# Kernel optimization log

Measured on AMD Instinct MI355X. Metric: run time of the kernel, lower is better.

Reference implementation:

```python
import jax, jax.numpy as jnp
import numpy as np

HIDDEN = 1024
HEADS = 16
HEAD_DIM = HIDDEN // HEADS
B, S = 4, 2048


def setup_inputs() -> dict:
    key = jax.random.key(0)
    ks = jax.random.split(key, 10)
    scale = 1.0 / np.sqrt(HIDDEN)
    def lin(k):
        return jax.random.uniform(k, (HIDDEN, HIDDEN), jnp.float32, -scale, scale)
    return {
        "x": jax.random.normal(ks[0], (B, S, HIDDEN), jnp.float32),
        "Wq": lin(ks[1]), "bq": jnp.zeros((HIDDEN,), jnp.float32),
        "Wk": lin(ks[2]), "bk": jnp.zeros((HIDDEN,), jnp.float32),
        "Wv": lin(ks[3]), "bv": jnp.zeros((HIDDEN,), jnp.float32),
        "Wo": lin(ks[4]), "bo": jnp.zeros((HIDDEN,), jnp.float32),
        "head_mask": jnp.ones((HEADS,), jnp.float32),
    }


def reference(x, Wq, bq, Wk, bk, Wv, bv, Wo, bo, head_mask):
    b, s, _ = x.shape
    # torch Linear: x @ W.T + b
    q = (x @ Wq.T + bq).reshape(b, s, HEADS, HEAD_DIM)
    k = (x @ Wk.T + bk).reshape(b, s, HEADS, HEAD_DIM)
    v = (x @ Wv.T + bv).reshape(b, s, HEADS, HEAD_DIM)
    # [b, h, s, s] attention scores
    attn = jnp.einsum("bqhd,bkhd->bhqk", q, k) / np.sqrt(HEAD_DIM).astype(np.float32)
    attn = jax.nn.softmax(attn, axis=-1)
    # post-softmax per-head mask scaling
    attn = attn * head_mask[None, :, None, None]
    out = jnp.einsum("bhqk,bkhd->bqhd", attn, v).reshape(b, s, HIDDEN)
    return out @ Wo.T + bo
```

## Files before the change

kernel.cpp:

```cpp
#include <hip/hip_runtime.h>
#include <hip/hip_bf16.h>

typedef __attribute__((ext_vector_type(8))) short bf16x8;
typedef __attribute__((ext_vector_type(4))) float f32x4;

#define SEQ 2048
#define NB 4
#define NH 16
#define HID 1024

__device__ __forceinline__ short f2bf(float f) {
  __hip_bfloat16 h = __float2bfloat16(f);
  union { __hip_bfloat16 h; short s; } u; u.h = h; return u.s;
}

__device__ __forceinline__ void gload_lds16(const void* g, void* l) {
  __builtin_amdgcn_global_load_lds((const __attribute__((address_space(1))) void*)g,
                                   (__attribute__((address_space(3))) void*)l, 16, 0, 0);
}

__global__ void cvt_f32_bf16(const float4* __restrict__ in, short4* __restrict__ out, int n4) {
  int i = blockIdx.x * 256 + threadIdx.x;
  if (i >= n4) return;
  float4 v = in[i];
  short4 o;
  o.x = f2bf(v.x); o.y = f2bf(v.y); o.z = f2bf(v.z); o.w = f2bf(v.w);
  out[i] = o;
}

template<int MODE>
__global__ __launch_bounds__(256, 2)
void gemm_bf16(const short* __restrict__ A,
               const short* __restrict__ B0, const short* __restrict__ B1, const short* __restrict__ B2,
               const float* __restrict__ bias0, const float* __restrict__ bias1, const float* __restrict__ bias2,
               short* __restrict__ o0, short* __restrict__ o1, short* __restrict__ o2,
               float* __restrict__ of) {
  __shared__ __align__(16) short As[128*64];
  __shared__ __align__(16) short Bs[128*64];
  const int tid = threadIdx.x;
  const int wave = tid >> 6, lane = tid & 63;
  const int lr = lane & 15, lk = lane >> 4;
  const int m0 = blockIdx.y * 128;
  const int n0 = blockIdx.x * 128;

  const short* Bm; const float* bias; int nloc; int proj = 0;
  if (MODE == 0) {
    proj = n0 >> 10;
    Bm   = proj == 0 ? B0 : (proj == 1 ? B1 : B2);
    bias = proj == 0 ? bias0 : (proj == 1 ? bias1 : bias2);
    nloc = n0 & 1023;
  } else { Bm = B0; bias = bias0; nloc = n0; }

  f32x4 acc[4][4];
  #pragma unroll
  for (int m = 0; m < 4; ++m)
    #pragma unroll
    for (int n = 0; n < 4; ++n) acc[m][n] = (f32x4){0.f,0.f,0.f,0.f};

  const int wr = (wave >> 1) * 64, wc = (wave & 1) * 64;

  for (int kt = 0; kt < 1024; kt += 64) {
    #pragma unroll
    for (int is = 0; is < 4; ++is) {
      int slot = is*256 + tid;
      int r = slot >> 3;
      int cs = (slot & 7) ^ (r & 7);
      gload_lds16(A  + (m0  + r)*1024 + kt + cs*8, As + (is*256 + wave*64)*8);
      gload_lds16(Bm + (nloc+ r)*1024 + kt + cs*8, Bs + (is*256 + wave*64)*8);
    }
    __syncthreads();
    #pragma unroll
    for (int kk = 0; kk < 2; ++kk) {
      bf16x8 av[4], bv[4];
      #pragma unroll
      for (int m = 0; m < 4; ++m) {
        int r = wr + m*16 + lr;
        av[m] = *(const bf16x8*)(As + (r*8 + ((kk*4 + lk) ^ (r & 7)))*8);
      }
      #pragma unroll
      for (int n = 0; n < 4; ++n) {
        int r = wc + n*16 + lr;
        bv[n] = *(const bf16x8*)(Bs + (r*8 + ((kk*4 + lk) ^ (r & 7)))*8);
      }
      #pragma unroll
      for (int m = 0; m < 4; ++m)
        #pragma unroll
        for (int n = 0; n < 4; ++n)
          acc[m][n] = __builtin_amdgcn_mfma_f32_16x16x32_bf16(av[m], bv[n], acc[m][n], 0, 0, 0);
    }
    __syncthreads();
  }

  if (MODE == 0) {
    if (proj < 2) {
      short* outp = proj == 0 ? o0 : o1;
      const float scale = (proj == 0) ? 0.125f : 1.0f;
      #pragma unroll
      for (int n = 0; n < 4; ++n) {
        int col = nloc + wc + n*16 + lr;
        int h = col >> 6, d = col & 63;
        float bvv = bias[col];
        #pragma unroll
        for (int m = 0; m < 4; ++m)
          #pragma unroll
          for (int j = 0; j < 4; ++j) {
            int row = m0 + wr + m*16 + lk*4 + j;
            int b = row >> 11, s = row & 2047;
            outp[(((b*NH + h)*SEQ + s) << 6) + d] = f2bf((acc[m][n][j] + bvv) * scale);
          }
      }
    } else {
      #pragma unroll
      for (int n = 0; n < 4; ++n) {
        int col = nloc + wc + n*16 + lr;
        int h = col >> 6, d = col & 63;
        float bvv = bias[col];
        #pragma unroll
        for (int m = 0; m < 4; ++m) {
          int row = m0 + wr + m*16 + lk*4;
          int b = row >> 11, s = row & 2047;
          short4 vv;
          vv.x = f2bf(acc[m][n][0] + bvv);
          vv.y = f2bf(acc[m][n][1] + bvv);
          vv.z = f2bf(acc[m][n][2] + bvv);
          vv.w = f2bf(acc[m][n][3] + bvv);
          *(short4*)(o2 + (((b*NH + h)*64 + d)*SEQ + s)) = vv;
        }
      }
    }
  } else {
    #pragma unroll
    for (int n = 0; n < 4; ++n) {
      int col = n0 + wc + n*16 + lr;
      float bvv = bias[col];
      #pragma unroll
      for (int m = 0; m < 4; ++m)
        #pragma unroll
        for (int j = 0; j < 4; ++j) {
          int row = m0 + wr + m*16 + lk*4 + j;
          of[row*HID + col] = acc[m][n][j] + bvv;
        }
    }
  }
}

__global__ __launch_bounds__(256, 2)
void attn_fwd(const short* __restrict__ Q, const short* __restrict__ K,
              const short* __restrict__ VT, const float* __restrict__ head_mask,
              short* __restrict__ O) {
  __shared__ __align__(16) short Ks[64*64];
  __shared__ __align__(16) short Vs[64*64];
  __shared__ __align__(16) short Ps[4][16*64];
  const int tid = threadIdx.x;
  const int wave = tid >> 6, lane = tid & 63;
  const int lr = lane & 15, lk = lane >> 4;
  const int bh = blockIdx.y;
  const int h = bh & (NH - 1);
  const int q0 = blockIdx.x * 64;
  const short* Qh = Q  + bh * SEQ * 64;
  const short* Kh = K  + bh * SEQ * 64;
  const short* Vh = VT + bh * 64 * SEQ;

  bf16x8 qf[2];
  {
    const short* qr = Qh + (q0 + wave*16 + lr)*64 + lk*8;
    qf[0] = *(const bf16x8*)qr;
    qf[1] = *(const bf16x8*)(qr + 32);
  }

  float row_m[4], row_l[4];
  f32x4 oacc[4];
  #pragma unroll
  for (int j = 0; j < 4; ++j) { row_m[j] = -1e30f; row_l[j] = 0.f; }
  #pragma unroll
  for (int n = 0; n < 4; ++n) oacc[n] = (f32x4){0.f,0.f,0.f,0.f};

  for (int kv0 = 0; kv0 < SEQ; kv0 += 64) {
    #pragma unroll
    for (int is = 0; is < 2; ++is) {
      int slot = is*256 + tid;
      int r = slot >> 3;
      int cs = (slot & 7) ^ (r & 7);
      gload_lds16(Kh + (kv0 + r)*64 + cs*8, Ks + (is*256 + wave*64)*8);
      gload_lds16(Vh + r*SEQ + kv0 + cs*8, Vs + (is*256 + wave*64)*8);
    }
    __syncthreads();

    f32x4 sc[4];
    #pragma unroll
    for (int n = 0; n < 4; ++n) sc[n] = (f32x4){0.f,0.f,0.f,0.f};
    #pragma unroll
    for (int kk = 0; kk < 2; ++kk)
      #pragma unroll
      for (int n = 0; n < 4; ++n) {
        int r = n*16 + lr;
        bf16x8 bv = *(const bf16x8*)(Ks + (r*8 + ((kk*4 + lk) ^ (r & 7)))*8);
        sc[n] = __builtin_amdgcn_mfma_f32_16x16x32_bf16(qf[kk], bv, sc[n], 0, 0, 0);
      }

    float pmax[4];
    #pragma unroll
    for (int j = 0; j < 4; ++j) {
      float v = fmaxf(fmaxf(sc[0][j], sc[1][j]), fmaxf(sc[2][j], sc[3][j]));
      v = fmaxf(v, __shfl_xor(v, 1));
      v = fmaxf(v, __shfl_xor(v, 2));
      v = fmaxf(v, __shfl_xor(v, 4));
      v = fmaxf(v, __shfl_xor(v, 8));
      pmax[j] = v;
    }
    float ps[4], rs[4];
    #pragma unroll
    for (int j = 0; j < 4; ++j) {
      float mn = fmaxf(row_m[j], pmax[j]);
      ps[j] = __expf(row_m[j] - mn);
      row_m[j] = mn;
      rs[j] = 0.f;
    }
    #pragma unroll
    for (int n = 0; n < 4; ++n)
      #pragma unroll
      for (int j = 0; j < 4; ++j) {
        float p = __expf(sc[n][j] - row_m[j]);
        sc[n][j] = p;
        rs[j] += p;
      }
    #pragma unroll
    for (int j = 0; j < 4; ++j) {
      float v = rs[j];
      v += __shfl_xor(v, 1);
      v += __shfl_xor(v, 2);
      v += __shfl_xor(v, 4);
      v += __shfl_xor(v, 8);
      row_l[j] = row_l[j]*ps[j] + v;
    }
    #pragma unroll
    for (int n = 0; n < 4; ++n)
      #pragma unroll
      for (int j = 0; j < 4; ++j) oacc[n][j] *= ps[j];

    short* Pw = Ps[wave];
    #pragma unroll
    for (int n = 0; n < 4; ++n)
      #pragma unroll
      for (int j = 0; j < 4; ++j) {
        int row = lk*4 + j;
        int col = n*16 + lr;
        int byteoff = row*128 + (((col >> 3) ^ (row >> 1))*16) + (col & 7)*2;
        *(short*)((char*)Pw + byteoff) = f2bf(sc[n][j]);
      }
    __syncthreads();

    #pragma unroll
    for (int kk = 0; kk < 2; ++kk) {
      bf16x8 av = *(const bf16x8*)(Pw + (lr*8 + ((kk*4 + lk) ^ (lr >> 1)))*8);
      #pragma unroll
      for (int n = 0; n < 4; ++n) {
        int r = n*16 + lr;
        bf16x8 bv = *(const bf16x8*)(Vs + (r*8 + ((kk*4 + lk) ^ (r & 7)))*8);
        oacc[n] = __builtin_amdgcn_mfma_f32_16x16x32_bf16(av, bv, oacc[n], 0, 0, 0);
      }
    }
    __syncthreads();
  }

  const float hm = head_mask[h];
  const int b = bh >> 4;
  #pragma unroll
  for (int j = 0; j < 4; ++j) {
    int q = q0 + wave*16 + lk*4 + j;
    float inv = hm / row_l[j];
    int rowbase = (b*SEQ + q)*HID + h*64;
    #pragma unroll
    for (int n = 0; n < 4; ++n)
      O[rowbase + n*16 + lr] = f2bf(oacc[n][j] * inv);
  }
}

extern "C" void kernel_launch(void* const* d_in, const int* in_sizes, int n_in,
                              void* d_out, int out_size, void* d_ws, size_t ws_size,
                              hipStream_t stream) {
  const float* x  = (const float*)d_in[0];
  const float* Wq = (const float*)d_in[1];
  const float* bq = (const float*)d_in[2];
  const float* Wk = (const float*)d_in[3];
  const float* bk = (const float*)d_in[4];
  const float* Wv = (const float*)d_in[5];
  const float* bv = (const float*)d_in[6];
  const float* Wo = (const float*)d_in[7];
  const float* bo = (const float*)d_in[8];
  const float* hm = (const float*)d_in[9];
  float* out = (float*)d_out;
  char* ws = (char*)d_ws;

  short* xb  = (short*)(ws);
  short* wqb = (short*)(ws + 16777216);
  short* wkb = (short*)(ws + 18874368);
  short* wvb = (short*)(ws + 20971520);
  short* wob = (short*)(ws + 23068672);
  short* Qb  = (short*)(ws + 25165824);
  short* Kb  = (short*)(ws + 41943040);
  short* Vb  = (short*)(ws + 58720256);
  short* AOb = (short*)(ws + 75497472);

  cvt_f32_bf16<<<8192, 256, 0, stream>>>((const float4*)x,  (short4*)xb,  2097152);
  cvt_f32_bf16<<<1024, 256, 0, stream>>>((const float4*)Wq, (short4*)wqb, 262144);
  cvt_f32_bf16<<<1024, 256, 0, stream>>>((const float4*)Wk, (short4*)wkb, 262144);
  cvt_f32_bf16<<<1024, 256, 0, stream>>>((const float4*)Wv, (short4*)wvb, 262144);
  cvt_f32_bf16<<<1024, 256, 0, stream>>>((const float4*)Wo, (short4*)wob, 262144);

  gemm_bf16<0><<<dim3(24, 64), 256, 0, stream>>>(xb, wqb, wkb, wvb, bq, bk, bv,
                                                 Qb, Kb, Vb, nullptr);
  attn_fwd<<<dim3(32, 64), 256, 0, stream>>>(Qb, Kb, Vb, hm, AOb);
  gemm_bf16<1><<<dim3(8, 64), 256, 0, stream>>>(AOb, wob, nullptr, nullptr, bo, nullptr, nullptr,
                                                nullptr, nullptr, nullptr, out);
}
```

Before: 392.5 us.

## Double-buffer K/V tiles, lazy softmax rescale, and drop intra-iteration barrier

K/V tiles are now double-buffered in LDS: the next tile's global-to-LDS load is issued before computing on the current one, so memory latency overlaps the MFMA work. The online softmax skips rescaling the accumulators unless some row max grows by more than 8 (wave-uniform check), which saves exp and multiply work. The barrier between the per-wave P store and the PV MFMA is removed, since each wave reads only its own P tile, and launch bounds rise to 4 blocks per CU. The extra LDS per block and the higher occupancy target could force register spills or limit residency, and the lazy rescale lets unnormalized values grow up to e^8.

```diff
diff --git a/kernel.cpp b/kernel.cpp
--- a/kernel.cpp
+++ b/kernel.cpp
@@ -144,12 +144,12 @@
   }
 }
 
-__global__ __launch_bounds__(256, 2)
+__global__ __launch_bounds__(256, 4)
 void attn_fwd(const short* __restrict__ Q, const short* __restrict__ K,
               const short* __restrict__ VT, const float* __restrict__ head_mask,
               short* __restrict__ O) {
-  __shared__ __align__(16) short Ks[64*64];
-  __shared__ __align__(16) short Vs[64*64];
+  __shared__ __align__(16) short Ks[2][64*64];
+  __shared__ __align__(16) short Vs[2][64*64];
   __shared__ __align__(16) short Ps[4][16*64];
   const int tid = threadIdx.x;
   const int wave = tid >> 6, lane = tid & 63;
@@ -161,6 +161,17 @@
   const short* Kh = K  + bh * SEQ * 64;
   const short* Vh = VT + bh * 64 * SEQ;
 
+  auto STAGE = [&](int buf, int kv0) {
+    #pragma unroll
+    for (int is = 0; is < 2; ++is) {
+      int slot = is*256 + tid;
+      int r = slot >> 3;
+      int cs = (slot & 7) ^ (r & 7);
+      gload_lds16(Kh + (kv0 + r)*64 + cs*8, Ks[buf] + (is*256 + wave*64)*8);
+      gload_lds16(Vh + r*SEQ + kv0 + cs*8, Vs[buf] + (is*256 + wave*64)*8);
+    }
+  };
+
   bf16x8 qf[2];
   {
     const short* qr = Qh + (q0 + wave*16 + lr)*64 + lk*8;
@@ -175,16 +186,13 @@
   #pragma unroll
   for (int n = 0; n < 4; ++n) oacc[n] = (f32x4){0.f,0.f,0.f,0.f};
 
-  for (int kv0 = 0; kv0 < SEQ; kv0 += 64) {
-    #pragma unroll
-    for (int is = 0; is < 2; ++is) {
-      int slot = is*256 + tid;
-      int r = slot >> 3;
-      int cs = (slot & 7) ^ (r & 7);
-      gload_lds16(Kh + (kv0 + r)*64 + cs*8, Ks + (is*256 + wave*64)*8);
-      gload_lds16(Vh + r*SEQ + kv0 + cs*8, Vs + (is*256 + wave*64)*8);
-    }
-    __syncthreads();
+  STAGE(0, 0);
+  __syncthreads();
+
+  const int NT = SEQ / 64;
+  for (int t = 0; t < NT; ++t) {
+    const int cur = t & 1;
+    if (t + 1 < NT) STAGE(cur ^ 1, (t + 1) * 64);
 
     f32x4 sc[4];
     #pragma unroll
@@ -194,7 +202,7 @@
       #pragma unroll
       for (int n = 0; n < 4; ++n) {
         int r = n*16 + lr;
-        bf16x8 bv = *(const bf16x8*)(Ks + (r*8 + ((kk*4 + lk) ^ (r & 7)))*8);
+        bf16x8 bv = *(const bf16x8*)(Ks[cur] + (r*8 + ((kk*4 + lk) ^ (r & 7)))*8);
         sc[n] = __builtin_amdgcn_mfma_f32_16x16x32_bf16(qf[kk], bv, sc[n], 0, 0, 0);
       }
 
@@ -208,14 +216,20 @@
       v = fmaxf(v, __shfl_xor(v, 8));
       pmax[j] = v;
     }
-    float ps[4], rs[4];
-    #pragma unroll
-    for (int j = 0; j < 4; ++j) {
-      float mn = fmaxf(row_m[j], pmax[j]);
-      ps[j] = __expf(row_m[j] - mn);
-      row_m[j] = mn;
-      rs[j] = 0.f;
-    }
+    bool ok = (pmax[0] <= row_m[0] + 8.f) && (pmax[1] <= row_m[1] + 8.f) &&
+              (pmax[2] <= row_m[2] + 8.f) && (pmax[3] <= row_m[3] + 8.f);
+    if (!__all(ok)) {
+      #pragma unroll
+      for (int j = 0; j < 4; ++j) {
+        float mn = fmaxf(row_m[j], pmax[j]);
+        float ps = __expf(row_m[j] - mn);
+        row_m[j] = mn;
+        row_l[j] *= ps;
+        #pragma unroll
+        for (int n = 0; n < 4; ++n) oacc[n][j] *= ps;
+      }
+    }
+    float rs[4] = {0.f, 0.f, 0.f, 0.f};
     #pragma unroll
     for (int n = 0; n < 4; ++n)
       #pragma unroll
@@ -231,12 +245,8 @@
       v += __shfl_xor(v, 2);
       v += __shfl_xor(v, 4);
       v += __shfl_xor(v, 8);
-      row_l[j] = row_l[j]*ps[j] + v;
-    }
-    #pragma unroll
-    for (int n = 0; n < 4; ++n)
-      #pragma unroll
-      for (int j = 0; j < 4; ++j) oacc[n][j] *= ps[j];
+      row_l[j] += v;
+    }
 
     short* Pw = Ps[wave];
     #pragma unroll
@@ -248,7 +258,6 @@
         int byteoff = row*128 + (((col >> 3) ^ (row >> 1))*16) + (col & 7)*2;
         *(short*)((char*)Pw + byteoff) = f2bf(sc[n][j]);
       }
-    __syncthreads();
 
     #pragma unroll
     for (int kk = 0; kk < 2; ++kk) {
@@ -256,7 +265,7 @@
       #pragma unroll
       for (int n = 0; n < 4; ++n) {
         int r = n*16 + lr;
-        bf16x8 bv = *(const bf16x8*)(Vs + (r*8 + ((kk*4 + lk) ^ (r & 7)))*8);
+        bf16x8 bv = *(const bf16x8*)(Vs[cur] + (r*8 + ((kk*4 + lk) ^ (r & 7)))*8);
         oacc[n] = __builtin_amdgcn_mfma_f32_16x16x32_bf16(av, bv, oacc[n], 0, 0, 0);
       }
     }
```

Result: slower. 416.3 us (+6.1%).

## Restructure attention with 32x32 MFMA, transposed scores, double-buffered KV, register P

Applied to the files above, without the earlier changes.

Rewrites the flash-attention kernel to process 128 query rows per block using 32x32x16 MFMAs, computing S^T so each lane owns one query row and softmax reductions become mostly in-register. K/V tiles are double-buffered in LDS and prefetched one tile ahead. P is repacked through lane shuffles instead of an LDS round trip, which drops one barrier per tile. Rescaling of the output accumulator is skipped unless the running max grows by more than 8. This adds register pressure and more complex lane mapping, and halves the grid size.

```diff
diff --git a/kernel.cpp b/kernel.cpp
--- a/kernel.cpp
+++ b/kernel.cpp
@@ -3,15 +3,22 @@
 
 typedef __attribute__((ext_vector_type(8))) short bf16x8;
 typedef __attribute__((ext_vector_type(4))) float f32x4;
+typedef __attribute__((ext_vector_type(16))) float f32x16;
+typedef unsigned int u32;
 
 #define SEQ 2048
 #define NB 4
 #define NH 16
 #define HID 1024
+#define QBLK 128
 
 __device__ __forceinline__ short f2bf(float f) {
   __hip_bfloat16 h = __float2bfloat16(f);
   union { __hip_bfloat16 h; short s; } u; u.h = h; return u.s;
+}
+
+__device__ __forceinline__ u32 pk2(float a, float b) {
+  return (u32)(unsigned short)f2bf(a) | ((u32)(unsigned short)f2bf(b) << 16);
 }
 
 __device__ __forceinline__ void gload_lds16(const void* g, void* l) {
@@ -144,135 +151,165 @@
   }
 }
 
-__global__ __launch_bounds__(256, 2)
+
+template<int BUF>
+__device__ __forceinline__ void attn_stage(int tid, int wave,
+                                           const short* __restrict__ Kh,
+                                           const short* __restrict__ Vh, int kv0,
+                                           short (&Ks)[2][64*64], short (&Vs)[2][64*64]) {
+  #pragma unroll
+  for (int is = 0; is < 2; ++is) {
+    int slot = is*256 + tid;
+    int r = slot >> 3;
+    int cs = (slot & 7) ^ (r & 7);
+    gload_lds16(Kh + (kv0 + r)*64 + cs*8, Ks[BUF] + (is*256 + wave*64)*8);
+    gload_lds16(Vh + r*SEQ + kv0 + cs*8, Vs[BUF] + (is*256 + wave*64)*8);
+  }
+}
+
+template<int CUR>
+__device__ __forceinline__ void attn_tile(int t, int NT, int tid, int wave, int qq, int hi,
+                                          const short* __restrict__ Kh,
+                                          const short* __restrict__ Vh,
+                                          short (&Ks)[2][64*64], short (&Vs)[2][64*64],
+                                          bf16x8 (&qf)[4], float& row_m, float& row_l,
+                                          f32x16 (&oacc)[2]) {
+  if (t + 1 < NT) attn_stage<CUR ^ 1>(tid, wave, Kh, Vh, (t + 1) * 64, Ks, Vs);
+
+  f32x16 sc[2];
+  #pragma unroll
+  for (int i = 0; i < 16; ++i) { sc[0][i] = 0.f; sc[1][i] = 0.f; }
+  #pragma unroll
+  for (int kb = 0; kb < 2; ++kb) {
+    int r = kb*32 + qq;
+    #pragma unroll
+    for (int ks = 0; ks < 4; ++ks) {
+      bf16x8 ka = *(const bf16x8*)(Ks[CUR] + (r*8 + ((ks*2 + hi) ^ (r & 7)))*8);
+      sc[kb] = __builtin_amdgcn_mfma_f32_32x32x16_bf16(ka, qf[ks], sc[kb], 0, 0, 0);
+    }
+  }
+
+  float tm[16];
+  #pragma unroll
+  for (int i = 0; i < 16; ++i) tm[i] = fmaxf(sc[0][i], sc[1][i]);
+  #pragma unroll
+  for (int s = 8; s >= 1; s >>= 1)
+    #pragma unroll
+    for (int i = 0; i < s; ++i) tm[i] = fmaxf(tm[i], tm[i + s]);
+  float mt = fmaxf(tm[0], __shfl_xor(tm[0], 32));
+
+  if (__any(mt > row_m + 8.f)) {
+    float mn = fmaxf(row_m, mt);
+    float ps = __expf(row_m - mn);
+    row_m = mn;
+    row_l *= ps;
+    #pragma unroll
+    for (int rg = 0; rg < 16; ++rg) {
+      int qsrc = (rg & 3) + 8*(rg >> 2) + 4*hi;
+      float po = __shfl(ps, qsrc);
+      oacc[0][rg] *= po;
+      oacc[1][rg] *= po;
+    }
+  }
+
+  #pragma unroll
+  for (int kb = 0; kb < 2; ++kb)
+    #pragma unroll
+    for (int i = 0; i < 16; ++i) sc[kb][i] = __expf(sc[kb][i] - row_m);
+
+  bf16x8 pa[4];
+  #pragma unroll
+  for (int ks = 0; ks < 4; ++ks) {
+    int kvb = ks >> 1;
+    int qe4 = (ks & 1) * 8;
+    u32 we0 = pk2(sc[kvb][qe4+0], sc[kvb][qe4+1]);
+    u32 we1 = pk2(sc[kvb][qe4+2], sc[kvb][qe4+3]);
+    u32 wo0 = pk2(sc[kvb][qe4+4], sc[kvb][qe4+5]);
+    u32 wo1 = pk2(sc[kvb][qe4+6], sc[kvb][qe4+7]);
+    u32 s0 = hi ? we0 : wo0;
+    u32 s1 = hi ? we1 : wo1;
+    u32 r0 = (u32)__shfl_xor((int)s0, 32);
+    u32 r1 = (u32)__shfl_xor((int)s1, 32);
+    u32 k0 = hi ? wo0 : we0;
+    u32 k1 = hi ? wo1 : we1;
+    union { u32 u[4]; bf16x8 v; } pu;
+    pu.u[0] = hi ? r0 : k0;
+    pu.u[1] = hi ? r1 : k1;
+    pu.u[2] = hi ? k0 : r0;
+    pu.u[3] = hi ? k1 : r1;
+    pa[ks] = pu.v;
+  }
+
+  #pragma unroll
+  for (int db = 0; db < 2; ++db) {
+    int r = db*32 + qq;
+    #pragma unroll
+    for (int ks = 0; ks < 4; ++ks) {
+      bf16x8 vb = *(const bf16x8*)(Vs[CUR] + (r*8 + ((ks*2 + hi) ^ (r & 7)))*8);
+      oacc[db] = __builtin_amdgcn_mfma_f32_32x32x16_bf16(pa[ks], vb, oacc[db], 0, 0, 0);
+    }
+  }
+
+  float ts[16];
+  #pragma unroll
+  for (int i = 0; i < 16; ++i) ts[i] = sc[0][i] + sc[1][i];
+  #pragma unroll
+  for (int s = 8; s >= 1; s >>= 1)
+    #pragma unroll
+    for (int i = 0; i < s; ++i) ts[i] += ts[i + s];
+  row_l += ts[0] + __shfl_xor(ts[0], 32);
+
+  __syncthreads();
+}
+
+__global__ __launch_bounds__(256, 3)
 void attn_fwd(const short* __restrict__ Q, const short* __restrict__ K,
               const short* __restrict__ VT, const float* __restrict__ head_mask,
               short* __restrict__ O) {
-  __shared__ __align__(16) short Ks[64*64];
-  __shared__ __align__(16) short Vs[64*64];
-  __shared__ __align__(16) short Ps[4][16*64];
+  __shared__ __align__(16) short Ks[2][64*64];
+  __shared__ __align__(16) short Vs[2][64*64];
   const int tid = threadIdx.x;
   const int wave = tid >> 6, lane = tid & 63;
-  const int lr = lane & 15, lk = lane >> 4;
+  const int qq = lane & 31;
+  const int hi = lane >> 5;
   const int bh = blockIdx.y;
   const int h = bh & (NH - 1);
-  const int q0 = blockIdx.x * 64;
+  const int q0 = blockIdx.x * QBLK;
   const short* Qh = Q  + bh * SEQ * 64;
   const short* Kh = K  + bh * SEQ * 64;
   const short* Vh = VT + bh * 64 * SEQ;
 
-  bf16x8 qf[2];
+  bf16x8 qf[4];
   {
-    const short* qr = Qh + (q0 + wave*16 + lr)*64 + lk*8;
-    qf[0] = *(const bf16x8*)qr;
-    qf[1] = *(const bf16x8*)(qr + 32);
-  }
-
-  float row_m[4], row_l[4];
-  f32x4 oacc[4];
-  #pragma unroll
-  for (int j = 0; j < 4; ++j) { row_m[j] = -1e30f; row_l[j] = 0.f; }
-  #pragma unroll
-  for (int n = 0; n < 4; ++n) oacc[n] = (f32x4){0.f,0.f,0.f,0.f};
-
-  for (int kv0 = 0; kv0 < SEQ; kv0 += 64) {
-    #pragma unroll
-    for (int is = 0; is < 2; ++is) {
-      int slot = is*256 + tid;
-      int r = slot >> 3;
-      int cs = (slot & 7) ^ (r & 7);
-      gload_lds16(Kh + (kv0 + r)*64 + cs*8, Ks + (is*256 + wave*64)*8);
-      gload_lds16(Vh + r*SEQ + kv0 + cs*8, Vs + (is*256 + wave*64)*8);
-    }
-    __syncthreads();
-
-    f32x4 sc[4];
-    #pragma unroll
-    for (int n = 0; n < 4; ++n) sc[n] = (f32x4){0.f,0.f,0.f,0.f};
-    #pragma unroll
-    for (int kk = 0; kk < 2; ++kk)
-      #pragma unroll
-      for (int n = 0; n < 4; ++n) {
-        int r = n*16 + lr;
-        bf16x8 bv = *(const bf16x8*)(Ks + (r*8 + ((kk*4 + lk) ^ (r & 7)))*8);
-        sc[n] = __builtin_amdgcn_mfma_f32_16x16x32_bf16(qf[kk], bv, sc[n], 0, 0, 0);
-      }
-
-    float pmax[4];
-    #pragma unroll
-    for (int j = 0; j < 4; ++j) {
-      float v = fmaxf(fmaxf(sc[0][j], sc[1][j]), fmaxf(sc[2][j], sc[3][j]));
-      v = fmaxf(v, __shfl_xor(v, 1));
-      v = fmaxf(v, __shfl_xor(v, 2));
-      v = fmaxf(v, __shfl_xor(v, 4));
-      v = fmaxf(v, __shfl_xor(v, 8));
-      pmax[j] = v;
-    }
-    float ps[4], rs[4];
-    #pragma unroll
-    for (int j = 0; j < 4; ++j) {
-      float mn = fmaxf(row_m[j], pmax[j]);
-      ps[j] = __expf(row_m[j] - mn);
-      row_m[j] = mn;
-      rs[j] = 0.f;
-    }
-    #pragma unroll
-    for (int n = 0; n < 4; ++n)
-      #pragma unroll
-      for (int j = 0; j < 4; ++j) {
-        float p = __expf(sc[n][j] - row_m[j]);
-        sc[n][j] = p;
-        rs[j] += p;
-      }
-    #pragma unroll
-    for (int j = 0; j < 4; ++j) {
-      float v = rs[j];
-      v += __shfl_xor(v, 1);
-      v += __shfl_xor(v, 2);
-      v += __shfl_xor(v, 4);
-      v += __shfl_xor(v, 8);
-      row_l[j] = row_l[j]*ps[j] + v;
-    }
-    #pragma unroll
-    for (int n = 0; n < 4; ++n)
-      #pragma unroll
-      for (int j = 0; j < 4; ++j) oacc[n][j] *= ps[j];
-
-    short* Pw = Ps[wave];
-    #pragma unroll
-    for (int n = 0; n < 4; ++n)
-      #pragma unroll
-      for (int j = 0; j < 4; ++j) {
-        int row = lk*4 + j;
-        int col = n*16 + lr;
-        int byteoff = row*128 + (((col >> 3) ^ (row >> 1))*16) + (col & 7)*2;
-        *(short*)((char*)Pw + byteoff) = f2bf(sc[n][j]);
-      }
-    __syncthreads();
-
-    #pragma unroll
-    for (int kk = 0; kk < 2; ++kk) {
-      bf16x8 av = *(const bf16x8*)(Pw + (lr*8 + ((kk*4 + lk) ^ (lr >> 1)))*8);
-      #pragma unroll
-      for (int n = 0; n < 4; ++n) {
-        int r = n*16 + lr;
-        bf16x8 bv = *(const bf16x8*)(Vs + (r*8 + ((kk*4 + lk) ^ (r & 7)))*8);
-        oacc[n] = __builtin_amdgcn_mfma_f32_16x16x32_bf16(av, bv, oacc[n], 0, 0, 0);
-      }
-    }
-    __syncthreads();
+    const short* qr = Qh + (q0 + wave*32 + qq)*64 + hi*8;
+    #pragma unroll
+    for (int ks = 0; ks < 4; ++ks) qf[ks] = *(const bf16x8*)(qr + ks*16);
+  }
+
+  float row_m = -1e30f, row_l = 0.f;
+  f32x16 oacc[2];
+  #pragma unroll
+  for (int i = 0; i < 16; ++i) { oacc[0][i] = 0.f; oacc[1][i] = 0.f; }
+
+  attn_stage<0>(tid, wave, Kh, Vh, 0, Ks, Vs);
+  __syncthreads();
+
+  const int NT = SEQ / 64;
+  for (int t = 0; t < NT; t += 2) {
+    attn_tile<0>(t,     NT, tid, wave, qq, hi, Kh, Vh, Ks, Vs, qf, row_m, row_l, oacc);
+    attn_tile<1>(t + 1, NT, tid, wave, qq, hi, Kh, Vh, Ks, Vs, qf, row_m, row_l, oacc);
   }
 
   const float hm = head_mask[h];
   const int b = bh >> 4;
-  #pragma unroll
-  for (int j = 0; j < 4; ++j) {
-    int q = q0 + wave*16 + lk*4 + j;
-    float inv = hm / row_l[j];
-    int rowbase = (b*SEQ + q)*HID + h*64;
-    #pragma unroll
-    for (int n = 0; n < 4; ++n)
-      O[rowbase + n*16 + lr] = f2bf(oacc[n][j] * inv);
+  float inv = hm / row_l;
+  #pragma unroll
+  for (int rg = 0; rg < 16; ++rg) {
+    int qsrc = (rg & 3) + 8*(rg >> 2) + 4*hi;
+    float io = __shfl(inv, qsrc);
+    int orow = (b*SEQ + q0 + wave*32 + qsrc)*HID + h*64;
+    O[orow + qq]      = f2bf(oacc[0][rg] * io);
+    O[orow + 32 + qq] = f2bf(oacc[1][rg] * io);
   }
 }
 
@@ -310,7 +347,7 @@
 
   gemm_bf16<0><<<dim3(24, 64), 256, 0, stream>>>(xb, wqb, wkb, wvb, bq, bk, bv,
                                                  Qb, Kb, Vb, nullptr);
-  attn_fwd<<<dim3(32, 64), 256, 0, stream>>>(Qb, Kb, Vb, hm, AOb);
+  attn_fwd<<<dim3(SEQ/QBLK, 64), 256, 0, stream>>>(Qb, Kb, Vb, hm, AOb);
   gemm_bf16<1><<<dim3(8, 64), 256, 0, stream>>>(AOb, wob, nullptr, nullptr, bo, nullptr, nullptr,
                                                 nullptr, nullptr, nullptr, out);
 }
```

After: 317.6 us. 1.24x faster.
